# Performance work log

Hardware: AMD Instinct MI355X
Metric: run time of the kernel (lower is better)

Reference implementation:

```python
import jax, jax.numpy as jnp
import numpy as np

D_MODEL = 2048
N_HEADS = 16
N_KV_HEADS = 4
HEAD_DIM = D_MODEL // N_HEADS  # 128
WINDOW = 512
SOFTCAP = 50.0
ROPE_THETA = 10000.0
BATCH = 2
SEQ = 2048
NEG_INF = -1e30


def _rope_cos_sin(seq_len, head_dim, theta):
    # inv_freq over half the head dim, duplicated (HF rotate_half convention)
    inv_freq = 1.0 / (theta ** (jnp.arange(0, head_dim, 2, dtype=jnp.float32) / head_dim))
    freqs = jnp.arange(seq_len, dtype=jnp.float32)[:, None] * inv_freq[None, :]  # [S, hd/2]
    emb = jnp.concatenate([freqs, freqs], axis=-1)  # [S, hd]
    return jnp.cos(emb), jnp.sin(emb)


def _rotate_half(x):
    x1, x2 = jnp.split(x, 2, axis=-1)
    return jnp.concatenate([-x2, x1], axis=-1)


def _apply_rope(x, cos, sin):
    # x: [B, S, H, hd]; cos/sin: [S, hd] broadcast over batch & heads (unsqueeze_dim=2)
    c = cos[None, :, None, :]
    s = sin[None, :, None, :]
    return x * c + _rotate_half(x) * s


def setup_inputs() -> dict:
    key = jax.random.key(0)
    ks = jax.random.split(key, 5)
    scale_p = 1.0 / np.sqrt(D_MODEL)
    return {
        "hidden_states": jax.random.normal(ks[0], (BATCH, SEQ, D_MODEL), dtype=jnp.float32),
        "wq": jax.random.normal(ks[1], (N_HEADS * HEAD_DIM, D_MODEL), dtype=jnp.float32) * scale_p,
        "wk": jax.random.normal(ks[2], (N_KV_HEADS * HEAD_DIM, D_MODEL), dtype=jnp.float32) * scale_p,
        "wv": jax.random.normal(ks[3], (N_KV_HEADS * HEAD_DIM, D_MODEL), dtype=jnp.float32) * scale_p,
        "wo": jax.random.normal(ks[4], (D_MODEL, N_HEADS * HEAD_DIM), dtype=jnp.float32) * scale_p,
    }


def reference(hidden_states, wq, wk, wv, wo):
    B, S, _ = hidden_states.shape
    groups = N_HEADS // N_KV_HEADS
    scale = HEAD_DIM ** -0.5

    q = (hidden_states @ wq.T).reshape(B, S, N_HEADS, HEAD_DIM)
    k = (hidden_states @ wk.T).reshape(B, S, N_KV_HEADS, HEAD_DIM)
    v = (hidden_states @ wv.T).reshape(B, S, N_KV_HEADS, HEAD_DIM)

    cos, sin = _rope_cos_sin(S, HEAD_DIM, ROPE_THETA)
    q = _apply_rope(q, cos, sin)
    k = _apply_rope(k, cos, sin)

    # GQA head expansion: each kv head serves `groups` query heads
    k = jnp.repeat(k, groups, axis=2)  # [B, S, H, hd]
    v = jnp.repeat(v, groups, axis=2)

    scores = jnp.einsum("bqhd,bkhd->bhqk", q, k) * scale
    scores = SOFTCAP * jnp.tanh(scores / SOFTCAP)

    i = jnp.arange(S)[:, None]
    j = jnp.arange(S)[None, :]
    allowed = (j <= i) & (j > i - WINDOW)  # causal + sliding window
    scores = jnp.where(allowed[None, None], scores, NEG_INF)

    attn = jax.nn.softmax(scores, axis=-1)
    out = jnp.einsum("bhqk,bkhd->bqhd", attn, v).reshape(B, S, N_HEADS * HEAD_DIM)
    return out @ wo.T
```

## Files before the change

kernel.cpp:

```cpp
#include <hip/hip_runtime.h>
#include <hip/hip_bf16.h>
#include <stdint.h>

#define DM    2048
#define NH    16
#define NKVH  4
#define HD    128
#define WIN   512
#define SEQL  2048
#define BAT   2
#define MR    (BAT*SEQL)
#define NQKV  3072
#define QKSCALE 0.08838834764831845f
#define CAP   50.0f
#define C1F (QKSCALE * 2.0f * 1.4426950408889634f / CAP)
#define C2F (-144.26950408889634f)

typedef unsigned short u16;
typedef __attribute__((ext_vector_type(8))) short short8;
typedef __attribute__((ext_vector_type(4))) float f32x4;

__device__ __forceinline__ u16 f2bf(float f) {
  union { float f; uint32_t u; } v; v.f = f;
  uint32_t r = v.u + 0x7FFFu + ((v.u >> 16) & 1u);
  return (u16)(r >> 16);
}
__device__ __forceinline__ float bf2f(u16 h) {
  union { uint32_t u; float f; } v; v.u = ((uint32_t)h) << 16; return v.f;
}
__device__ __forceinline__ void gld16(const void* g, void* l) {
  __builtin_amdgcn_global_load_lds((const __attribute__((address_space(1))) void*)g,
                                   (__attribute__((address_space(3))) void*)l,
                                   16, 0, 0);
}
__device__ __forceinline__ float exp_softcap(float sv) {
  float t = __builtin_amdgcn_exp2f(sv);
  float u = __builtin_amdgcn_rcpf(t + 1.0f);
  return __builtin_amdgcn_exp2f(u * C2F);
}

__global__ void k_cast(const float* __restrict__ src, u16* __restrict__ dst, int n4) {
  int i = blockIdx.x * 256 + threadIdx.x;
  if (i >= n4) return;
  float4 v = ((const float4*)src)[i];
  ushort4 o;
  o.x = f2bf(v.x); o.y = f2bf(v.y); o.z = f2bf(v.z); o.w = f2bf(v.w);
  ((ushort4*)dst)[i] = o;
}

__global__ void k_rope_table(float* __restrict__ c, float* __restrict__ sn) {
  int s = blockIdx.x, i = threadIdx.x;
  float invf = expf(-(float)i * (9.210340371976184f / 64.0f));
  float a = (float)s * invf;
  c[(s << 6) + i]  = cosf(a);
  sn[(s << 6) + i] = sinf(a);
}

template <typename OutT>
__global__ __launch_bounds__(256, 3) void k_gemm_bt(const u16* __restrict__ A,
                                                    const u16* __restrict__ Bm,
                                                    OutT* __restrict__ C,
                                                    int N, int K) {
  __shared__ __align__(16) u16 ldsA[128 * 64];
  __shared__ __align__(16) u16 ldsB[128 * 64];
  const int t = threadIdx.x;

  const int nwg  = gridDim.x * gridDim.y;
  const int flat = blockIdx.y * gridDim.x + blockIdx.x;
  const int cpx  = nwg >> 3;
  const int swz  = (flat & 7) * cpx + (flat >> 3);
  const int bn = swz % gridDim.x, bm = swz / gridDim.x;

  const int m0 = bm * 128, n0 = bn * 128;
  const int lane = t & 63, wid = t >> 6;
  const int lr = lane & 15, lk = lane >> 4;
  const int wr = (wid >> 1) * 64, wc = (wid & 1) * 64;
  const int nt = K >> 6;

  const int srow = t >> 3;
  const int scol = (((t & 7) ^ (srow & 7)) << 3);

  f32x4 acc[4][4];
  #pragma unroll
  for (int mi = 0; mi < 4; ++mi)
    #pragma unroll
    for (int ni = 0; ni < 4; ++ni) acc[mi][ni] = f32x4{0.f, 0.f, 0.f, 0.f};

  for (int kt = 0; kt < nt; ++kt) {
    {
      const u16* a0 = A  + (size_t)(m0 + srow) * K + kt * 64 + scol;
      const u16* b0 = Bm + (size_t)(n0 + srow) * K + kt * 64 + scol;
      #pragma unroll
      for (int i = 0; i < 4; ++i) {
        gld16(a0 + (size_t)(i * 32) * K, &ldsA[i * 2048 + t * 8]);
        gld16(b0 + (size_t)(i * 32) * K, &ldsB[i * 2048 + t * 8]);
      }
    }
    __syncthreads();
    #pragma unroll
    for (int ks = 0; ks < 2; ++ks) {
      const int c = ks * 4 + lk;
      short8 af[4], bfv[4];
      #pragma unroll
      for (int mi = 0; mi < 4; ++mi) {
        const int ra = wr + mi * 16 + lr;
        af[mi] = *(const short8*)(ldsA + ra * 64 + ((c ^ (ra & 7)) << 3));
      }
      #pragma unroll
      for (int ni = 0; ni < 4; ++ni) {
        const int rb = wc + ni * 16 + lr;
        bfv[ni] = *(const short8*)(ldsB + rb * 64 + ((c ^ (rb & 7)) << 3));
      }
      #pragma unroll
      for (int mi = 0; mi < 4; ++mi)
        #pragma unroll
        for (int ni = 0; ni < 4; ++ni)
          acc[mi][ni] = __builtin_amdgcn_mfma_f32_16x16x32_bf16(af[mi], bfv[ni], acc[mi][ni], 0, 0, 0);
    }
    if (kt + 1 < nt) __syncthreads();
  }

  #pragma unroll
  for (int mi = 0; mi < 4; ++mi) {
    #pragma unroll
    for (int ni = 0; ni < 4; ++ni) {
      const int r0 = m0 + wr + mi * 16 + lk * 4;
      const int c  = n0 + wc + ni * 16 + lr;
      #pragma unroll
      for (int r = 0; r < 4; ++r) {
        float v = acc[mi][ni][r];
        if constexpr (__is_same(OutT, float)) C[(size_t)(r0 + r) * N + c] = v;
        else                                  C[(size_t)(r0 + r) * N + c] = f2bf(v);
      }
    }
  }
}

__global__ void k_rope_q(const u16* __restrict__ C, const float* __restrict__ cosT,
                         const float* __restrict__ sinT, u16* __restrict__ qr) {
  int idx = blockIdx.x * 256 + threadIdx.x;
  int i = idx & 63, hh = (idx >> 6) & 15, m = idx >> 10;
  int s = m & (SEQL - 1), b = m >> 11;
  size_t cb = (size_t)m * NQKV + hh * HD + i;
  float x1 = bf2f(C[cb]), x2 = bf2f(C[cb + 64]);
  float c = cosT[(s << 6) + i], sn = sinT[(s << 6) + i];
  size_t ob = ((size_t)(b * NH + hh) * SEQL + s) * HD + i;
  qr[ob]      = f2bf((x1 * c - x2 * sn) * C1F);
  qr[ob + 64] = f2bf((x2 * c + x1 * sn) * C1F);
}

__global__ void k_rope_k(const u16* __restrict__ C, const float* __restrict__ cosT,
                         const float* __restrict__ sinT, u16* __restrict__ kr) {
  int idx = blockIdx.x * 256 + threadIdx.x;
  int i = idx & 63, kvh = (idx >> 6) & 3, m = idx >> 8;
  int s = m & (SEQL - 1), b = m >> 11;
  size_t cb = (size_t)m * NQKV + 2048 + kvh * HD + i;
  float x1 = bf2f(C[cb]), x2 = bf2f(C[cb + 64]);
  float c = cosT[(s << 6) + i], sn = sinT[(s << 6) + i];
  size_t ob = ((size_t)(b * NKVH + kvh) * SEQL + s) * HD + i;
  kr[ob]      = f2bf(x1 * c - x2 * sn);
  kr[ob + 64] = f2bf(x2 * c + x1 * sn);
}

__global__ void k_vt(const u16* __restrict__ C, u16* __restrict__ vt) {
  int idx = blockIdx.x * 256 + threadIdx.x;
  int s = idx & (SEQL - 1);
  int d = (idx >> 11) & 127;
  int kvh = (idx >> 18) & 3;
  int b = idx >> 20;
  int m = b * SEQL + s;
  vt[idx] = C[(size_t)m * NQKV + 2560 + kvh * HD + d];
}

__global__ __launch_bounds__(256, 4) void k_attn(const u16* __restrict__ qr,
                                                 const u16* __restrict__ kr,
                                                 const u16* __restrict__ vt,
                                                 u16* __restrict__ ao) {
  __shared__ __align__(16) u16 kbuf[2][32 * 128];
  __shared__ __align__(16) u16 vbuf[2][128 * 32];
  __shared__ __align__(16) u16 plds[4][16 * 40];

  const int t = threadIdx.x;
  const int wid = t >> 6, lane = t & 63, lr = lane & 15, lk = lane >> 4;
  const int h = blockIdx.x, bq = blockIdx.y, b = blockIdx.z;
  const int kvh = h >> 2;
  const int Q0 = bq * 64;
  const int q0w = Q0 + wid * 16;
  const u16* qb = qr + (size_t)(b * NH + h) * SEQL * HD;
  const u16* kb = kr + (size_t)(b * NKVH + kvh) * SEQL * HD;
  const u16* vb = vt + (size_t)(b * NKVH + kvh) * HD * SEQL;

  short8 qf[4];
  #pragma unroll
  for (int kc = 0; kc < 4; ++kc)
    qf[kc] = *(const short8*)(qb + (size_t)(q0w + lr) * HD + kc * 32 + lk * 8);

  f32x4 o[8];
  #pragma unroll
  for (int dt = 0; dt < 8; ++dt) o[dt] = f32x4{0.f, 0.f, 0.f, 0.f};
  float lsum = 0.f;

  int lo = Q0 - (WIN - 1); if (lo < 0) lo = 0;
  const int ktlo = lo >> 5, kthi = (Q0 + 63) >> 5;

  auto stageK = [&](int bufi, int kv0) {
    #pragma unroll
    for (int i = 0; i < 2; ++i) {
      int c = t + i * 256;
      int bb = c << 4;
      int sb = bb ^ (((bb >> 8) & 7) << 4);
      gld16(kb + (size_t)(kv0 + (sb >> 8)) * HD + ((sb & 255) >> 1),
            &kbuf[bufi][c << 3]);
    }
  };
  auto stageV = [&](int bufi, int kv0) {
    #pragma unroll
    for (int i = 0; i < 2; ++i) {
      int c = t + i * 256;
      int bb = c << 4;
      int sb = bb ^ (((bb >> 7) & 3) << 4);
      gld16(vb + (size_t)(sb >> 6) * SEQL + kv0 + ((sb & 63) >> 1),
            &vbuf[bufi][c << 3]);
    }
  };

  stageK(0, ktlo << 5);
  stageV(0, ktlo << 5);
  __syncthreads();

  u16* pw = plds[wid];

  for (int kt = ktlo; kt <= kthi; ++kt) {
    const int cur = kt & 1;
    if (kt < kthi) { stageK(cur ^ 1, (kt + 1) << 5); stageV(cur ^ 1, (kt + 1) << 5); }
    const int kv0 = kt << 5;
    if (kv0 + 31 >= q0w - (WIN - 1) && kv0 <= q0w + 15) {
      f32x4 sv0 = f32x4{0.f, 0.f, 0.f, 0.f}, sv1 = sv0;
      const u16* lks = kbuf[cur];
      #pragma unroll
      for (int kc = 0; kc < 4; ++kc) {
        int b0 = (lr * 256 + kc * 64 + lk * 16) ^ ((lr & 7) << 4);
        int b1 = ((lr + 16) * 256 + kc * 64 + lk * 16) ^ ((lr & 7) << 4);
        short8 k0 = *(const short8*)(lks + (b0 >> 1));
        short8 k1 = *(const short8*)(lks + (b1 >> 1));
        sv0 = __builtin_amdgcn_mfma_f32_16x16x32_bf16(k0, qf[kc], sv0, 0, 0, 0);
        sv1 = __builtin_amdgcn_mfma_f32_16x16x32_bf16(k1, qf[kc], sv1, 0, 0, 0);
      }
      float p[8];
      #pragma unroll
      for (int r = 0; r < 4; ++r) {
        p[r]     = exp_softcap(sv0[r]);
        p[r + 4] = exp_softcap(sv1[r]);
      }
      const bool interior = (kv0 + 31 <= q0w) && (kv0 >= q0w + 16 - WIN);
      if (!interior) {
        const int qg = q0w + lr;
        #pragma unroll
        for (int r = 0; r < 4; ++r) {
          int kg0 = kv0 + lk * 4 + r, kg1 = kg0 + 16;
          if (!(kg0 <= qg && kg0 > qg - WIN)) p[r] = 0.f;
          if (!(kg1 <= qg && kg1 > qg - WIN)) p[r + 4] = 0.f;
        }
      }
      lsum += ((p[0] + p[1]) + (p[2] + p[3])) + ((p[4] + p[5]) + (p[6] + p[7]));
      __hip_bfloat162 u0 = __float22bfloat162_rn(float2{p[0], p[1]});
      __hip_bfloat162 u1 = __float22bfloat162_rn(float2{p[2], p[3]});
      __hip_bfloat162 u2 = __float22bfloat162_rn(float2{p[4], p[5]});
      __hip_bfloat162 u3 = __float22bfloat162_rn(float2{p[6], p[7]});
      uint2 w0; w0.x = *(uint32_t*)&u0; w0.y = *(uint32_t*)&u1;
      uint2 w1; w1.x = *(uint32_t*)&u2; w1.y = *(uint32_t*)&u3;
      *(uint2*)(pw + lr * 40 + lk * 4)      = w0;
      *(uint2*)(pw + lr * 40 + 16 + lk * 4) = w1;
      short8 pf = *(const short8*)(pw + lr * 40 + lk * 8);
      const u16* lvs = vbuf[cur];
      #pragma unroll
      for (int dt = 0; dt < 8; ++dt) {
        int row = dt * 16 + lr;
        int bb = (row * 64 + lk * 16) ^ (((row >> 1) & 3) << 4);
        o[dt] = __builtin_amdgcn_mfma_f32_16x16x32_bf16(pf, *(const short8*)(lvs + (bb >> 1)), o[dt], 0, 0, 0);
      }
    }
    __syncthreads();
  }

  lsum += __shfl_xor(lsum, 16);
  lsum += __shfl_xor(lsum, 32);
  float linv = 1.0f / lsum;
  #pragma unroll
  for (int r = 0; r < 4; ++r) {
    float inv = __shfl(linv, lk * 4 + r);
    const int srow = q0w + lk * 4 + r;
    u16* op = ao + (size_t)(b * SEQL + srow) * DM + h * HD;
    #pragma unroll
    for (int dt = 0; dt < 8; ++dt) op[dt * 16 + lr] = f2bf(o[dt][r] * inv);
  }
}

extern "C" void kernel_launch(void* const* d_in, const int* in_sizes, int n_in,
                              void* d_out, int out_size, void* d_ws, size_t ws_size,
                              hipStream_t stream) {
  (void)in_sizes; (void)n_in; (void)out_size; (void)ws_size;
  const float* hs = (const float*)d_in[0];
  const float* wq = (const float*)d_in[1];
  const float* wk = (const float*)d_in[2];
  const float* wv = (const float*)d_in[3];
  const float* wo = (const float*)d_in[4];
  float* out = (float*)d_out;

  u16* ws    = (u16*)d_ws;
  u16* A_bf  = ws;
  u16* Wqkv  = A_bf + 8388608;
  u16* Cqkv  = Wqkv + 6291456;
  u16* q_r   = Cqkv + 12582912;
  u16* k_r   = q_r + 8388608;
  u16* vTb   = k_r + 2097152;
  float* cosT = (float*)(vTb + 2097152);
  float* sinT = cosT + 131072;
  u16* Wo   = Cqkv;
  u16* aout = A_bf;

  k_cast<<<8192, 256, 0, stream>>>(hs, A_bf, 2097152);
  k_cast<<<4096, 256, 0, stream>>>(wq, Wqkv, 1048576);
  k_cast<<<1024, 256, 0, stream>>>(wk, Wqkv + 4194304, 262144);
  k_cast<<<1024, 256, 0, stream>>>(wv, Wqkv + 5242880, 262144);
  k_rope_table<<<2048, 64, 0, stream>>>(cosT, sinT);

  k_gemm_bt<u16><<<dim3(NQKV / 128, MR / 128), 256, 0, stream>>>(A_bf, Wqkv, Cqkv, NQKV, DM);

  k_rope_q<<<16384, 256, 0, stream>>>(Cqkv, cosT, sinT, q_r);
  k_rope_k<<<4096, 256, 0, stream>>>(Cqkv, cosT, sinT, k_r);
  k_vt<<<8192, 256, 0, stream>>>(Cqkv, vTb);
  k_cast<<<4096, 256, 0, stream>>>(wo, Wo, 1048576);

  k_attn<<<dim3(NH, SEQL / 64, BAT), 256, 0, stream>>>(q_r, k_r, vTb, aout);

  k_gemm_bt<float><<<dim3(DM / 128, MR / 128), 256, 0, stream>>>(aout, Wo, out, DM, DM);
}
```

Measured before the change: 189.4 us.

## Switch attention to 32x32x16 MFMA with 128-row query tiles

The attention kernel now uses 32x32x16 bf16 MFMA instead of 16x16x32, with each wave handling 32 query rows and each block 128 rows. The P matrix is moved into the A-operand layout through cross-lane shuffles rather than a round trip through LDS. The goal is to raise reuse of each staged K/V tile, cut LDS traffic and remove the P staging buffer. In exchange the grid has half as many blocks, register use per thread is higher (launch bounds drop to 2 blocks per unit), and more tiles need masking along the window edges.

```diff
diff --git a/kernel.cpp b/kernel.cpp
--- a/kernel.cpp
+++ b/kernel.cpp
@@ -19,6 +19,7 @@
 typedef unsigned short u16;
 typedef __attribute__((ext_vector_type(8))) short short8;
 typedef __attribute__((ext_vector_type(4))) float f32x4;
+typedef __attribute__((ext_vector_type(16))) float f32x16;
 
 __device__ __forceinline__ u16 f2bf(float f) {
   union { float f; uint32_t u; } v; v.f = f;
@@ -172,36 +173,38 @@
   vt[idx] = C[(size_t)m * NQKV + 2560 + kvh * HD + d];
 }
 
-__global__ __launch_bounds__(256, 4) void k_attn(const u16* __restrict__ qr,
+__global__ __launch_bounds__(256, 2) void k_attn(const u16* __restrict__ qr,
                                                  const u16* __restrict__ kr,
                                                  const u16* __restrict__ vt,
                                                  u16* __restrict__ ao) {
   __shared__ __align__(16) u16 kbuf[2][32 * 128];
   __shared__ __align__(16) u16 vbuf[2][128 * 32];
-  __shared__ __align__(16) u16 plds[4][16 * 40];
 
   const int t = threadIdx.x;
-  const int wid = t >> 6, lane = t & 63, lr = lane & 15, lk = lane >> 4;
+  const int wid = t >> 6, lane = t & 63;
+  const int l31 = lane & 31, lh = lane >> 5;
   const int h = blockIdx.x, bq = blockIdx.y, b = blockIdx.z;
   const int kvh = h >> 2;
-  const int Q0 = bq * 64;
-  const int q0w = Q0 + wid * 16;
+  const int Q0 = bq * 128;
+  const int q0w = Q0 + wid * 32;
   const u16* qb = qr + (size_t)(b * NH + h) * SEQL * HD;
   const u16* kb = kr + (size_t)(b * NKVH + kvh) * SEQL * HD;
   const u16* vb = vt + (size_t)(b * NKVH + kvh) * HD * SEQL;
 
-  short8 qf[4];
-  #pragma unroll
-  for (int kc = 0; kc < 4; ++kc)
-    qf[kc] = *(const short8*)(qb + (size_t)(q0w + lr) * HD + kc * 32 + lk * 8);
-
-  f32x4 o[8];
-  #pragma unroll
-  for (int dt = 0; dt < 8; ++dt) o[dt] = f32x4{0.f, 0.f, 0.f, 0.f};
+  short8 qf[8];
+  #pragma unroll
+  for (int ks = 0; ks < 8; ++ks)
+    qf[ks] = *(const short8*)(qb + (size_t)(q0w + l31) * HD + ks * 16 + lh * 8);
+
+  f32x16 o[4];
+  #pragma unroll
+  for (int dt = 0; dt < 4; ++dt)
+    #pragma unroll
+    for (int i = 0; i < 16; ++i) o[dt][i] = 0.f;
   float lsum = 0.f;
 
   int lo = Q0 - (WIN - 1); if (lo < 0) lo = 0;
-  const int ktlo = lo >> 5, kthi = (Q0 + 63) >> 5;
+  const int ktlo = lo >> 5, kthi = (Q0 + 127) >> 5;
 
   auto stageK = [&](int bufi, int kv0) {
     #pragma unroll
@@ -228,71 +231,85 @@
   stageV(0, ktlo << 5);
   __syncthreads();
 
-  u16* pw = plds[wid];
-
   for (int kt = ktlo; kt <= kthi; ++kt) {
     const int cur = kt & 1;
     if (kt < kthi) { stageK(cur ^ 1, (kt + 1) << 5); stageV(cur ^ 1, (kt + 1) << 5); }
     const int kv0 = kt << 5;
-    if (kv0 + 31 >= q0w - (WIN - 1) && kv0 <= q0w + 15) {
-      f32x4 sv0 = f32x4{0.f, 0.f, 0.f, 0.f}, sv1 = sv0;
+    if (kv0 + 31 >= q0w - (WIN - 1) && kv0 <= q0w + 31) {
+      f32x16 sv;
+      #pragma unroll
+      for (int i = 0; i < 16; ++i) sv[i] = 0.f;
       const u16* lks = kbuf[cur];
       #pragma unroll
-      for (int kc = 0; kc < 4; ++kc) {
-        int b0 = (lr * 256 + kc * 64 + lk * 16) ^ ((lr & 7) << 4);
-        int b1 = ((lr + 16) * 256 + kc * 64 + lk * 16) ^ ((lr & 7) << 4);
-        short8 k0 = *(const short8*)(lks + (b0 >> 1));
-        short8 k1 = *(const short8*)(lks + (b1 >> 1));
-        sv0 = __builtin_amdgcn_mfma_f32_16x16x32_bf16(k0, qf[kc], sv0, 0, 0, 0);
-        sv1 = __builtin_amdgcn_mfma_f32_16x16x32_bf16(k1, qf[kc], sv1, 0, 0, 0);
-      }
-      float p[8];
-      #pragma unroll
-      for (int r = 0; r < 4; ++r) {
-        p[r]     = exp_softcap(sv0[r]);
-        p[r + 4] = exp_softcap(sv1[r]);
-      }
-      const bool interior = (kv0 + 31 <= q0w) && (kv0 >= q0w + 16 - WIN);
-      if (!interior) {
-        const int qg = q0w + lr;
+      for (int ks = 0; ks < 8; ++ks) {
+        int bo = (l31 * 256 + ks * 32 + lh * 16) ^ ((l31 & 7) << 4);
+        short8 kf = *(const short8*)(lks + (bo >> 1));
+        sv = __builtin_amdgcn_mfma_f32_32x32x16_bf16(kf, qf[ks], sv, 0, 0, 0);
+      }
+      float p[16];
+      const bool interior = (kv0 + 31 <= q0w) && (kv0 >= q0w + 32 - WIN);
+      if (interior) {
         #pragma unroll
-        for (int r = 0; r < 4; ++r) {
-          int kg0 = kv0 + lk * 4 + r, kg1 = kg0 + 16;
-          if (!(kg0 <= qg && kg0 > qg - WIN)) p[r] = 0.f;
-          if (!(kg1 <= qg && kg1 > qg - WIN)) p[r + 4] = 0.f;
+        for (int r = 0; r < 16; ++r) p[r] = exp_softcap(sv[r]);
+      } else {
+        const int qg = q0w + l31;
+        #pragma unroll
+        for (int r = 0; r < 16; ++r) {
+          const int kg = kv0 + (r & 3) + 8 * (r >> 2) + 4 * lh;
+          float e = exp_softcap(sv[r]);
+          p[r] = (kg <= qg && kg > qg - WIN) ? e : 0.f;
         }
       }
-      lsum += ((p[0] + p[1]) + (p[2] + p[3])) + ((p[4] + p[5]) + (p[6] + p[7]));
-      __hip_bfloat162 u0 = __float22bfloat162_rn(float2{p[0], p[1]});
-      __hip_bfloat162 u1 = __float22bfloat162_rn(float2{p[2], p[3]});
-      __hip_bfloat162 u2 = __float22bfloat162_rn(float2{p[4], p[5]});
-      __hip_bfloat162 u3 = __float22bfloat162_rn(float2{p[6], p[7]});
-      uint2 w0; w0.x = *(uint32_t*)&u0; w0.y = *(uint32_t*)&u1;
-      uint2 w1; w1.x = *(uint32_t*)&u2; w1.y = *(uint32_t*)&u3;
-      *(uint2*)(pw + lr * 40 + lk * 4)      = w0;
-      *(uint2*)(pw + lr * 40 + 16 + lk * 4) = w1;
-      short8 pf = *(const short8*)(pw + lr * 40 + lk * 8);
+      #pragma unroll
+      for (int r = 0; r < 16; ++r) lsum += p[r];
+
+      uint32_t w[8];
+      #pragma unroll
+      for (int r2 = 0; r2 < 8; ++r2) {
+        __hip_bfloat162 u = __float22bfloat162_rn(float2{p[2 * r2], p[2 * r2 + 1]});
+        w[r2] = *(uint32_t*)&u;
+      }
+      uint32_t z0 = lh ? w[0] : w[2], z1 = lh ? w[1] : w[3];
+      uint32_t z2 = lh ? w[4] : w[6], z3 = lh ? w[5] : w[7];
+      uint32_t x0 = __shfl_xor((int)z0, 32), x1 = __shfl_xor((int)z1, 32);
+      uint32_t x2 = __shfl_xor((int)z2, 32), x3 = __shfl_xor((int)z3, 32);
+      union U8 { uint32_t u[4]; short8 s; };
+      U8 pa0, pa1;
+      pa0.u[0] = lh ? x0 : w[0];  pa0.u[1] = lh ? x1 : w[1];
+      pa0.u[2] = lh ? w[2] : x0;  pa0.u[3] = lh ? w[3] : x1;
+      pa1.u[0] = lh ? x2 : w[4];  pa1.u[1] = lh ? x3 : w[5];
+      pa1.u[2] = lh ? w[6] : x2;  pa1.u[3] = lh ? w[7] : x3;
+
       const u16* lvs = vbuf[cur];
       #pragma unroll
-      for (int dt = 0; dt < 8; ++dt) {
-        int row = dt * 16 + lr;
-        int bb = (row * 64 + lk * 16) ^ (((row >> 1) & 3) << 4);
-        o[dt] = __builtin_amdgcn_mfma_f32_16x16x32_bf16(pf, *(const short8*)(lvs + (bb >> 1)), o[dt], 0, 0, 0);
+      for (int ks2 = 0; ks2 < 2; ++ks2) {
+        const short8 paf = ks2 ? pa1.s : pa0.s;
+        #pragma unroll
+        for (int dt = 0; dt < 4; ++dt) {
+          int row = dt * 32 + l31;
+          int bo = (row * 64 + ks2 * 32 + lh * 16) ^ (((row >> 1) & 3) << 4);
+          short8 vf = *(const short8*)(lvs + (bo >> 1));
+          o[dt] = __builtin_amdgcn_mfma_f32_32x32x16_bf16(paf, vf, o[dt], 0, 0, 0);
+        }
       }
     }
     __syncthreads();
   }
 
-  lsum += __shfl_xor(lsum, 16);
   lsum += __shfl_xor(lsum, 32);
   float linv = 1.0f / lsum;
   #pragma unroll
-  for (int r = 0; r < 4; ++r) {
-    float inv = __shfl(linv, lk * 4 + r);
-    const int srow = q0w + lk * 4 + r;
-    u16* op = ao + (size_t)(b * SEQL + srow) * DM + h * HD;
-    #pragma unroll
-    for (int dt = 0; dt < 8; ++dt) op[dt * 16 + lr] = f2bf(o[dt][r] * inv);
+  for (int rr = 0; rr < 4; ++rr) {
+    #pragma unroll
+    for (int r = 0; r < 4; ++r) {
+      const int crow = r + 8 * rr + 4 * lh;
+      float inv = __shfl(linv, crow);
+      const int srow = q0w + crow;
+      u16* op = ao + (size_t)(b * SEQL + srow) * DM + h * HD;
+      #pragma unroll
+      for (int dt = 0; dt < 4; ++dt)
+        op[dt * 32 + l31] = f2bf(o[dt][rr * 4 + r] * inv);
+    }
   }
 }
 
@@ -332,7 +349,7 @@
   k_vt<<<8192, 256, 0, stream>>>(Cqkv, vTb);
   k_cast<<<4096, 256, 0, stream>>>(wo, Wo, 1048576);
 
-  k_attn<<<dim3(NH, SEQL / 64, BAT), 256, 0, stream>>>(q_r, k_r, vTb, aout);
+  k_attn<<<dim3(NH, SEQL / 128, BAT), 256, 0, stream>>>(q_r, k_r, vTb, aout);
 
   k_gemm_bt<float><<<dim3(DM / 128, MR / 128), 256, 0, stream>>>(aout, Wo, out, DM, DM);
 }
```

Result: no change. 189.9 us (+0.3%).
